# Performance work log

Hardware: AMD Instinct MI355X
Metric: run time of the kernel (lower is better)

Reference implementation:

```python
import jax, jax.numpy as jnp
import numpy as np

NUM_ATOMS = 100
D = 32        # initial_atom_dim
H = 16        # hidden_dim (multiplicity per irrep)
NB = 16       # edge_dim / number of bessel basis functions
CUT = 6.0     # radius_cutoff
DEG = 4.0     # degree_norm
OUT = 1       # output_dim
INV4PI = 1.0 / np.sqrt(4.0 * np.pi)  # 'integral' SH normalization


def _bessel(d, nb, cut):
    # e3nn soft_one_hot_linspace(basis='bessel', cutoff=True) * sqrt(nb)
    x = d[:, None]
    n = jnp.arange(1, nb + 1, dtype=d.dtype)
    safe = jnp.maximum(x, 1e-9)
    out = np.sqrt(2.0 / cut) * jnp.sin(n * jnp.pi * x / cut) / safe
    return out * (x < cut) * np.sqrt(float(nb))


def _fc(x, w1, w2):
    # e3nn FullyConnectedNet: fan-in normalized linear layers, silu, no bias
    h = jax.nn.silu(x @ w1 / np.sqrt(x.shape[-1]))
    return h @ w2 / np.sqrt(w1.shape[-1])


def _forward(atomic_numbers, edge_index, coords, atom_emb,
             fc0_w1, fc0_w2, fc1_w1, fc1_w2, w_readout):
    src, dst = edge_index[0], edge_index[1]
    N = coords.shape[0]
    E = src.shape[0]

    vec = coords[src] - coords[dst]                      # [E,3]
    dist = jnp.linalg.norm(vec, axis=-1)                 # [E]
    unit = vec / jnp.maximum(dist, 1e-9)[:, None]

    # spherical harmonics, l=0 and l=1, 'integral' normalization
    y0 = jnp.full((E,), INV4PI, dtype=coords.dtype)      # [E]
    y1 = (np.sqrt(3.0) * INV4PI) * unit                  # [E,3]
    basis = _bessel(dist, NB, CUT)                       # [E,NB]

    x = atom_emb[atomic_numbers]                         # [N,D] (row 0 is padding)

    # ---- layer 0: scalars (D x0e) x (1x0e+1x1o) -> H x0e + H x1o ----
    w = _fc(basis, fc0_w1, fc0_w2)                       # [E, 2*D*H] per-edge TP weights
    wa = w[:, : D * H].reshape(E, D, H)
    wb = w[:, D * H:].reshape(E, D, H)
    xs = x[src]
    n0 = 1.0 / np.sqrt(D)                                # path fan-in norm
    m0 = jnp.einsum('ed,edh->eh', xs, wa) * y0[:, None] * n0          # [E,H]
    m1 = jnp.einsum('ed,edh->eh', xs, wb)[:, :, None] * y1[:, None, :] * n0  # [E,H,3]
    z0 = jax.ops.segment_sum(m0, dst, num_segments=N) / DEG           # [N,H]
    z1 = jax.ops.segment_sum(m1, dst, num_segments=N) / DEG           # [N,H,3]

    # ---- layer 1: (H x0e + H x1o) x (1x0e+1x1o) -> same irreps, skip-connected ----
    w = _fc(basis, fc1_w1, fc1_w2)                       # [E, 4*H*H]
    w1_ = w[:, 0 * H * H:1 * H * H].reshape(E, H, H)     # 0e x 0e -> 0e
    w2_ = w[:, 1 * H * H:2 * H * H].reshape(E, H, H)     # 0e x 1o -> 1o
    w3_ = w[:, 2 * H * H:3 * H * H].reshape(E, H, H)     # 1o x 0e -> 1o
    w4_ = w[:, 3 * H * H:4 * H * H].reshape(E, H, H)     # 1o x 1o -> 0e (CG = dot/sqrt(3))
    s, v = z0[src], z1[src]
    n1 = 1.0 / np.sqrt(2 * H)                            # two paths per output irrep
    dot = jnp.einsum('ehm,em->eh', v, y1) / np.sqrt(3.0)
    o0 = (jnp.einsum('eh,ehk->ek', s, w1_) * y0[:, None]
          + jnp.einsum('eh,ehk->ek', dot, w4_)) * n1
    o1 = (jnp.einsum('eh,ehk->ek', s, w2_)[:, :, None] * y1[:, None, :]
          + jnp.einsum('ehm,ehk->ekm', v, w3_) * y0[:, None, None]) * n1
    z0 = jax.ops.segment_sum(o0, dst, num_segments=N) / DEG + z0      # skip
    z1 = jax.ops.segment_sum(o1, dst, num_segments=N) / DEG + z1

    # ---- scalar readout (o3.Linear onto 0e) + graph sum-pool ----
    node_scalar = z0 @ w_readout / np.sqrt(H)            # [N,OUT]
    return jnp.sum(node_scalar, axis=0)                  # [OUT]


def setup_inputs() -> dict:
    key = jax.random.key(0)
    ks = jax.random.split(key, 9)
    N, E = 10000, 160000
    atomic_numbers = jax.random.randint(ks[0], (N,), 0, NUM_ATOMS)
    coords = jax.random.normal(ks[1], (N, 3), dtype=jnp.float32)
    edge_index = jax.random.randint(ks[2], (2, E), 0, N)
    atom_emb = jax.random.normal(ks[3], (NUM_ATOMS, D), dtype=jnp.float32).at[0].set(0.0)
    fc0_w1 = jax.random.normal(ks[4], (NB, H), dtype=jnp.float32)
    fc0_w2 = jax.random.normal(ks[5], (H, 2 * D * H), dtype=jnp.float32)
    fc1_w1 = jax.random.normal(ks[6], (NB, H), dtype=jnp.float32)
    fc1_w2 = jax.random.normal(ks[7], (H, 4 * H * H), dtype=jnp.float32)
    w_readout = jax.random.normal(ks[8], (H, OUT), dtype=jnp.float32)
    return {"atomic_numbers": atomic_numbers, "coords": coords, "edge_index": edge_index,
            "atom_emb": atom_emb, "fc0_w1": fc0_w1, "fc0_w2": fc0_w2,
            "fc1_w1": fc1_w1, "fc1_w2": fc1_w2, "w_readout": w_readout}


def reference(atomic_numbers, coords, edge_index, atom_emb,
              fc0_w1, fc0_w2, fc1_w1, fc1_w2, w_readout):
    return _forward(atomic_numbers, edge_index, coords, atom_emb,
                    fc0_w1, fc0_w2, fc1_w1, fc1_w2, w_readout)
```

## Files before the change

kernel.cpp:

```cpp
#include <hip/hip_runtime.h>
#include <math.h>


namespace {
constexpr int   NATOMS   = 100;
constexpr int   CAP      = 64;
constexpr float PI_F     = 3.14159265358979323846f;
constexpr float INV4PI_F = 0.28209479177387814f;
constexpr float SQRT3_F  = 1.7320508075688772f;
constexpr float CUT_F    = 6.0f;
constexpr float BASIS_C  = 2.3094010767585034f;
constexpr float N0_F     = 0.17677669529663687f;
constexpr float K0_F = INV4PI_F * N0_F * 0.0625f;
constexpr float K1_F = SQRT3_F * INV4PI_F * N0_F * 0.0625f;
constexpr float P2SC = INV4PI_F * N0_F * (1.0f / 64.0f);
}

__device__ __forceinline__ float silu_fast(float x) {
  return x / (1.0f + __expf(-x));
}

__device__ __forceinline__ float block_reduce_sum(float v) {
  #pragma unroll
  for (int o = 32; o > 0; o >>= 1) v += __shfl_down(v, o, 64);
  __shared__ float ls[8];
  int lane = threadIdx.x & 63;
  int w    = threadIdx.x >> 6;
  if (lane == 0) ls[w] = v;
  __syncthreads();
  float s = 0.f;
  if (threadIdx.x == 0) {
    int nw = (blockDim.x + 63) >> 6;
    for (int i = 0; i < nw; ++i) s += ls[i];
  }
  return s;
}

__global__ void table_kernel(const float* __restrict__ atom_emb,
                             const float* __restrict__ fc0_w2,
                             const float* __restrict__ fc1_w2,
                             const float* __restrict__ w_readout,
                             float* __restrict__ TI,
                             float* __restrict__ G1T, float* __restrict__ G4T) {
  int b = blockIdx.x;
  int tt = threadIdx.x;
  int j = tt >> 4;
  int h = tt & 15;
  if (b < NATOMS) {
    float s0 = 0.f, s1 = 0.f;
    #pragma unroll
    for (int d = 0; d < 32; ++d) {
      float x = atom_emb[b * 32 + d];
      s0 = fmaf(x, fc0_w2[j * 1024 + d * 16 + h], s0);
      s1 = fmaf(x, fc0_w2[j * 1024 + 512 + d * 16 + h], s1);
    }
    TI[b * 512 + j * 32 + 2 * h]     = s0;
    TI[b * 512 + j * 32 + 2 * h + 1] = s1;
  } else {
    float g1 = 0.f, g4 = 0.f;
    #pragma unroll
    for (int k = 0; k < 16; ++k) {
      float r = w_readout[k];
      g1 = fmaf(fc1_w2[j * 1024 + h * 16 + k], r, g1);
      g4 = fmaf(fc1_w2[j * 1024 + 768 + h * 16 + k], r, g4);
    }
    G1T[h * 16 + j] = g1;
    G4T[h * 16 + j] = g4;
  }
}

__global__ void __launch_bounds__(256)
edge_kernel(const int* __restrict__ ei,
            const float* __restrict__ coords,
            const int* __restrict__ an,
            const float* __restrict__ TI,
            const float* __restrict__ fc0_w1,
            const float* __restrict__ fc1_w1,
            int* __restrict__ dcur, int* __restrict__ scur,
            float2* __restrict__ mbuf,
            float4* __restrict__ ubuf,
            float4* __restrict__ sbuf,
            float* __restrict__ hbuf,
            int E) {
  int lane = threadIdx.x & 63;
  int g    = threadIdx.x >> 4;
  int t    = threadIdx.x & 15;
  int base = lane & 48;

  float w0c[16], w1c[16];
  #pragma unroll
  for (int k = 0; k < 16; ++k) {
    w0c[k] = fc0_w1[k * 16 + t];
    w1c[k] = fc1_w1[k * 16 + t];
  }

  const float angc = PI_F / CUT_F;
  int e = blockIdx.x * 32 + g;
  #pragma unroll
  for (int rep = 0; rep < 2; ++rep, e += 16) {
    if (e < E) {
      int s = ei[e];
      int d = ei[E + e];
      float vx = coords[3 * s + 0] - coords[3 * d + 0];
      float vy = coords[3 * s + 1] - coords[3 * d + 1];
      float vz = coords[3 * s + 2] - coords[3 * d + 2];
      float dist = sqrtf(vx * vx + vy * vy + vz * vz);
      float inv  = 1.0f / fmaxf(dist, 1e-9f);
      float ux = vx * inv, uy = vy * inv, uz = vz * inv;
      float bc = (dist < CUT_F) ? (BASIS_C * inv) : 0.0f;

      int dslotv = 0, sslotv = 0;
      if (t == 0) {
        float4 rec = make_float4(ux, uy, uz, dist);
        int pos  = atomicAdd(&dcur[d], 1);
        int spos = atomicAdd(&scur[s], 1);
        int dslot = d * CAP + min(pos, CAP - 1);
        int sslot = s * CAP + min(spos, CAP - 1);
        ubuf[dslot] = rec;
        sbuf[sslot] = rec;
        dslotv = dslot; sslotv = sslot;
      }
      int dslot = __shfl(dslotv, base, 64);
      int sslot = __shfl(sslotv, base, 64);

      float ang = angc * dist;
      float sc0 = __sinf(ang);
      float tw  = 2.0f * __cosf(ang);
      float sc1 = sc0;
      float sp0 = 0.f, sp1 = 0.f, acc0 = 0.f, acc1 = 0.f;
      #pragma unroll
      for (int k = 0; k < 16; ++k) {
        acc0 = fmaf(sc0, w0c[k], acc0);
        acc1 = fmaf(sc1, w1c[k], acc1);
        float sn0 = fmaf(tw, sc0, -sp0); sp0 = sc0; sc0 = sn0;
        float sn1 = fmaf(tw, sc1, -sp1); sp1 = sc1; sc1 = sn1;
      }
      float h0t = silu_fast(acc0 * bc * 0.25f);
      float h1t = silu_fast(acc1 * bc * 0.25f);

      hbuf[(size_t)sslot * 16 + t] = h1t;

      int a = an[s];
      const float2* tp = (const float2*)(TI + a * 512) + t;
      float u0 = 0.f, u1 = 0.f;
      #pragma unroll
      for (int j = 0; j < 16; ++j) {
        float hj = __shfl(h0t, base + j, 64);
        float2 T = tp[j * 16];
        u0 = fmaf(hj, T.x, u0);
        u1 = fmaf(hj, T.y, u1);
      }
      mbuf[(size_t)dslot * 16 + t] = make_float2(K0_F * u0, K1_F * u1);
    }
  }
}

__global__ void __launch_bounds__(256, 4)
node_kernel(const int* __restrict__ dcur,
            const int* __restrict__ scur,
            const float2* __restrict__ mbuf,
            const float4* __restrict__ ubuf,
            const float4* __restrict__ sbuf,
            const float* __restrict__ hbuf,
            const float* __restrict__ G1T,
            const float* __restrict__ G4T,
            const float* __restrict__ w_readout,
            float* __restrict__ out,
            int N) {
  __shared__ float ggs[512];
  ggs[threadIdx.x]       = G1T[threadIdx.x];
  ggs[256 + threadIdx.x] = G4T[threadIdx.x];
  __syncthreads();

  int wave = threadIdx.x >> 6;
  int lane = threadIdx.x & 63;
  int g    = lane >> 4;
  int t    = lane & 15;
  int base = lane & 48;
  int node = blockIdx.x * 4 + wave;
  bool valid = node < N;

  float rr = w_readout[t];
  int cin  = valid ? min(dcur[node], CAP) : 0;
  int cout = valid ? min(scur[node], CAP) : 0;
  size_t nb = (size_t)(valid ? node : 0) * CAP;

  float a0 = 0.f, ax = 0.f, ay = 0.f, az = 0.f;
  for (int i = g; i < cin; i += 4) {
    float2 f  = mbuf[(nb + i) * 16 + t];
    float4 uu = ubuf[nb + i];
    a0 += f.x;
    ax = fmaf(f.y, uu.x, ax);
    ay = fmaf(f.y, uu.y, ay);
    az = fmaf(f.y, uu.z, az);
  }
  a0 += __shfl_xor(a0, 16, 64); a0 += __shfl_xor(a0, 32, 64);
  ax += __shfl_xor(ax, 16, 64); ax += __shfl_xor(ax, 32, 64);
  ay += __shfl_xor(ay, 16, 64); ay += __shfl_xor(ay, 32, 64);
  az += __shfl_xor(az, 16, 64); az += __shfl_xor(az, 32, 64);

  float srcv = (g == 0) ? a0 : ((g == 1) ? ax : (g == 2) ? ay : az);
  int tofs = (g == 0) ? 0 : 256;
  float o = 0.f;
  #pragma unroll
  for (int h = 0; h < 16; ++h) {
    float vh = __shfl(srcv, base + h, 64);
    o = fmaf(ggs[tofs + h * 16 + t], vh, o);
  }
  float Qt  = __shfl(o, t, 64);
  float Pxt = __shfl(o, 16 + t, 64);
  float Pyt = __shfl(o, 32 + t, 64);
  float Pzt = __shfl(o, 48 + t, 64);

  float c = 0.f;
  for (int i = g; i < cout; i += 4) {
    float h1 = hbuf[(nb + i) * 16 + t];
    float4 uu = sbuf[nb + i];
    c = fmaf(h1, fmaf(Pxt, uu.x, fmaf(Pyt, uu.y, fmaf(Pzt, uu.z, Qt))), c);
  }
  c *= P2SC;
  if (valid && g == 0) c = fmaf(a0 * rr, 0.25f, c);
  if (!valid) c = 0.f;

  float tot = block_reduce_sum(c);
  if (threadIdx.x == 0) atomicAdd(out, tot);
}

extern "C" void kernel_launch(void* const* d_in, const int* in_sizes, int n_in,
                              void* d_out, int out_size, void* d_ws, size_t ws_size,
                              hipStream_t stream) {
  const int*   an        = (const int*)d_in[0];
  const float* coords    = (const float*)d_in[1];
  const int*   ei        = (const int*)d_in[2];
  const float* atom_emb  = (const float*)d_in[3];
  const float* fc0_w1    = (const float*)d_in[4];
  const float* fc0_w2    = (const float*)d_in[5];
  const float* fc1_w1    = (const float*)d_in[6];
  const float* fc1_w2    = (const float*)d_in[7];
  const float* w_readout = (const float*)d_in[8];

  int N = in_sizes[0];
  int E = in_sizes[2] / 2;
  size_t slots = (size_t)N * CAP;

  float4* ubuf = (float4*)d_ws;
  float4* sbuf = ubuf + slots;
  float2* mbuf = (float2*)(sbuf + slots);
  float*  hbuf = (float*)(mbuf + slots * 16);
  float*  TI   = hbuf + slots * 16;
  float*  G1T  = TI + NATOMS * 512;
  float*  G4T  = G1T + 256;
  int*    dcur = (int*)(G4T + 256);
  int*    scur = dcur + N;
  float*  out = (float*)d_out;

  hipMemsetAsync(dcur, 0, (size_t)2 * N * sizeof(int), stream);
  hipMemsetAsync(out, 0, sizeof(float), stream);

  int blk = 256;
  table_kernel<<<NATOMS + 1, blk, 0, stream>>>(
      atom_emb, fc0_w2, fc1_w2, w_readout, TI, G1T, G4T);

  edge_kernel<<<(E + 31) / 32, blk, 0, stream>>>(
      ei, coords, an, TI, fc0_w1, fc1_w1, dcur, scur,
      mbuf, ubuf, sbuf, hbuf, E);

  node_kernel<<<(N + 3) / 4, blk, 0, stream>>>(
      dcur, scur, mbuf, ubuf, sbuf, hbuf, G1T, G4T, w_readout, out, N);
}
```

Measured before the change: 150.9 us.

## Fold memsets into table kernel and interleave two edges per thread

Removes the two hipMemsetAsync calls by having extra blocks of the table kernel zero the per-node counters and the output scalar, which saves launch overhead. The edge kernel is restructured so each thread issues the loads, atomics and math for both of its edges together instead of looping over them one at a time. This exposes more memory-level parallelism and hides gather latency, at the cost of more registers per thread.

```diff
diff --git a/kernel.cpp b/kernel.cpp
--- a/kernel.cpp
+++ b/kernel.cpp
@@ -41,12 +41,15 @@
                              const float* __restrict__ fc1_w2,
                              const float* __restrict__ w_readout,
                              float* __restrict__ TI,
-                             float* __restrict__ G1T, float* __restrict__ G4T) {
+                             float* __restrict__ G1T, float* __restrict__ G4T,
+                             int* __restrict__ dcur,
+                             float* __restrict__ out,
+                             int N2) {
   int b = blockIdx.x;
   int tt = threadIdx.x;
-  int j = tt >> 4;
-  int h = tt & 15;
   if (b < NATOMS) {
+    int j = tt >> 4;
+    int h = tt & 15;
     float s0 = 0.f, s1 = 0.f;
     #pragma unroll
     for (int d = 0; d < 32; ++d) {
@@ -56,7 +59,9 @@
     }
     TI[b * 512 + j * 32 + 2 * h]     = s0;
     TI[b * 512 + j * 32 + 2 * h + 1] = s1;
-  } else {
+  } else if (b == NATOMS) {
+    int j = tt >> 4;
+    int h = tt & 15;
     float g1 = 0.f, g4 = 0.f;
     #pragma unroll
     for (int k = 0; k < 16; ++k) {
@@ -66,6 +71,10 @@
     }
     G1T[h * 16 + j] = g1;
     G4T[h * 16 + j] = g4;
+    if (tt == 0) *out = 0.f;
+  } else {
+    int idx = (b - NATOMS - 1) * 256 + tt;
+    if (idx < N2) dcur[idx] = 0;
   }
 }
 
@@ -95,63 +104,93 @@
   }
 
   const float angc = PI_F / CUT_F;
-  int e = blockIdx.x * 32 + g;
-  #pragma unroll
-  for (int rep = 0; rep < 2; ++rep, e += 16) {
-    if (e < E) {
-      int s = ei[e];
-      int d = ei[E + e];
-      float vx = coords[3 * s + 0] - coords[3 * d + 0];
-      float vy = coords[3 * s + 1] - coords[3 * d + 1];
-      float vz = coords[3 * s + 2] - coords[3 * d + 2];
-      float dist = sqrtf(vx * vx + vy * vy + vz * vz);
-      float inv  = 1.0f / fmaxf(dist, 1e-9f);
-      float ux = vx * inv, uy = vy * inv, uz = vz * inv;
-      float bc = (dist < CUT_F) ? (BASIS_C * inv) : 0.0f;
-
-      int dslotv = 0, sslotv = 0;
-      if (t == 0) {
-        float4 rec = make_float4(ux, uy, uz, dist);
-        int pos  = atomicAdd(&dcur[d], 1);
-        int spos = atomicAdd(&scur[s], 1);
-        int dslot = d * CAP + min(pos, CAP - 1);
-        int sslot = s * CAP + min(spos, CAP - 1);
-        ubuf[dslot] = rec;
-        sbuf[sslot] = rec;
-        dslotv = dslot; sslotv = sslot;
-      }
-      int dslot = __shfl(dslotv, base, 64);
-      int sslot = __shfl(sslotv, base, 64);
-
-      float ang = angc * dist;
-      float sc0 = __sinf(ang);
-      float tw  = 2.0f * __cosf(ang);
-      float sc1 = sc0;
-      float sp0 = 0.f, sp1 = 0.f, acc0 = 0.f, acc1 = 0.f;
-      #pragma unroll
-      for (int k = 0; k < 16; ++k) {
-        acc0 = fmaf(sc0, w0c[k], acc0);
-        acc1 = fmaf(sc1, w1c[k], acc1);
-        float sn0 = fmaf(tw, sc0, -sp0); sp0 = sc0; sc0 = sn0;
-        float sn1 = fmaf(tw, sc1, -sp1); sp1 = sc1; sc1 = sn1;
-      }
-      float h0t = silu_fast(acc0 * bc * 0.25f);
-      float h1t = silu_fast(acc1 * bc * 0.25f);
-
-      hbuf[(size_t)sslot * 16 + t] = h1t;
-
-      int a = an[s];
-      const float2* tp = (const float2*)(TI + a * 512) + t;
-      float u0 = 0.f, u1 = 0.f;
-      #pragma unroll
-      for (int j = 0; j < 16; ++j) {
-        float hj = __shfl(h0t, base + j, 64);
-        float2 T = tp[j * 16];
-        u0 = fmaf(hj, T.x, u0);
-        u1 = fmaf(hj, T.y, u1);
-      }
-      mbuf[(size_t)dslot * 16 + t] = make_float2(K0_F * u0, K1_F * u1);
+  int eA = blockIdx.x * 32 + g;
+  int eB = eA + 16;
+  bool vA = eA < E, vB = eB < E;
+  int eAc = vA ? eA : 0, eBc = vB ? eB : 0;
+
+  int sA = ei[eAc], dA = ei[E + eAc];
+  int sB = ei[eBc], dB = ei[E + eBc];
+  float sxA = coords[3 * sA + 0], syA = coords[3 * sA + 1], szA = coords[3 * sA + 2];
+  float dxA = coords[3 * dA + 0], dyA = coords[3 * dA + 1], dzA = coords[3 * dA + 2];
+  float sxB = coords[3 * sB + 0], syB = coords[3 * sB + 1], szB = coords[3 * sB + 2];
+  float dxB = coords[3 * dB + 0], dyB = coords[3 * dB + 1], dzB = coords[3 * dB + 2];
+  int aA = an[sA], aB = an[sB];
+
+  float vxA = sxA - dxA, vyA = syA - dyA, vzA = szA - dzA;
+  float vxB = sxB - dxB, vyB = syB - dyB, vzB = szB - dzB;
+  float distA = sqrtf(vxA * vxA + vyA * vyA + vzA * vzA);
+  float distB = sqrtf(vxB * vxB + vyB * vyB + vzB * vzB);
+  float ivA = 1.0f / fmaxf(distA, 1e-9f);
+  float ivB = 1.0f / fmaxf(distB, 1e-9f);
+  float uxA = vxA * ivA, uyA = vyA * ivA, uzA = vzA * ivA;
+  float uxB = vxB * ivB, uyB = vyB * ivB, uzB = vzB * ivB;
+  float bcA = (distA < CUT_F) ? (BASIS_C * ivA) : 0.0f;
+  float bcB = (distB < CUT_F) ? (BASIS_C * ivB) : 0.0f;
+
+  int dsAv = 0, ssAv = 0, dsBv = 0, ssBv = 0;
+  if (t == 0) {
+    if (vA) {
+      int p = atomicAdd(&dcur[dA], 1), q = atomicAdd(&scur[sA], 1);
+      dsAv = dA * CAP + min(p, CAP - 1);
+      ssAv = sA * CAP + min(q, CAP - 1);
+      ubuf[dsAv] = make_float4(uxA, uyA, uzA, distA);
+      sbuf[ssAv] = make_float4(uxA, uyA, uzA, distA);
     }
+    if (vB) {
+      int p = atomicAdd(&dcur[dB], 1), q = atomicAdd(&scur[sB], 1);
+      dsBv = dB * CAP + min(p, CAP - 1);
+      ssBv = sB * CAP + min(q, CAP - 1);
+      ubuf[dsBv] = make_float4(uxB, uyB, uzB, distB);
+      sbuf[ssBv] = make_float4(uxB, uyB, uzB, distB);
+    }
+  }
+
+  float angA = angc * distA, angB = angc * distB;
+  float scA = __sinf(angA), twA = 2.0f * __cosf(angA), spA = 0.f;
+  float scB = __sinf(angB), twB = 2.0f * __cosf(angB), spB = 0.f;
+  float a0A = 0.f, a1A = 0.f, a0B = 0.f, a1B = 0.f;
+  #pragma unroll
+  for (int k = 0; k < 16; ++k) {
+    a0A = fmaf(scA, w0c[k], a0A);
+    a1A = fmaf(scA, w1c[k], a1A);
+    a0B = fmaf(scB, w0c[k], a0B);
+    a1B = fmaf(scB, w1c[k], a1B);
+    float snA = fmaf(twA, scA, -spA); spA = scA; scA = snA;
+    float snB = fmaf(twB, scB, -spB); spB = scB; scB = snB;
+  }
+  float h0A = silu_fast(a0A * bcA * 0.25f);
+  float h1A = silu_fast(a1A * bcA * 0.25f);
+  float h0B = silu_fast(a0B * bcB * 0.25f);
+  float h1B = silu_fast(a1B * bcB * 0.25f);
+
+  int dsA = __shfl(dsAv, base, 64);
+  int ssA = __shfl(ssAv, base, 64);
+  int dsB = __shfl(dsBv, base, 64);
+  int ssB = __shfl(ssBv, base, 64);
+
+  const float2* tpA = (const float2*)(TI + aA * 512) + t;
+  const float2* tpB = (const float2*)(TI + aB * 512) + t;
+  float u0A = 0.f, u1A = 0.f, u0B = 0.f, u1B = 0.f;
+  #pragma unroll
+  for (int j = 0; j < 16; ++j) {
+    float hjA = __shfl(h0A, base + j, 64);
+    float hjB = __shfl(h0B, base + j, 64);
+    float2 TA = tpA[j * 16];
+    float2 TB = tpB[j * 16];
+    u0A = fmaf(hjA, TA.x, u0A);
+    u1A = fmaf(hjA, TA.y, u1A);
+    u0B = fmaf(hjB, TB.x, u0B);
+    u1B = fmaf(hjB, TB.y, u1B);
+  }
+
+  if (vA) {
+    hbuf[(size_t)ssA * 16 + t] = h1A;
+    mbuf[(size_t)dsA * 16 + t] = make_float2(K0_F * u0A, K1_F * u1A);
+  }
+  if (vB) {
+    hbuf[(size_t)ssB * 16 + t] = h1B;
+    mbuf[(size_t)dsB * 16 + t] = make_float2(K0_F * u0B, K1_F * u1B);
   }
 }
 
@@ -254,12 +293,10 @@
   int*    scur = dcur + N;
   float*  out = (float*)d_out;
 
-  hipMemsetAsync(dcur, 0, (size_t)2 * N * sizeof(int), stream);
-  hipMemsetAsync(out, 0, sizeof(float), stream);
-
   int blk = 256;
-  table_kernel<<<NATOMS + 1, blk, 0, stream>>>(
-      atom_emb, fc0_w2, fc1_w2, w_readout, TI, G1T, G4T);
+  int zgrid = (2 * N + blk - 1) / blk;
+  table_kernel<<<NATOMS + 1 + zgrid, blk, 0, stream>>>(
+      atom_emb, fc0_w2, fc1_w2, w_readout, TI, G1T, G4T, dcur, out, 2 * N);
 
   edge_kernel<<<(E + 31) / 32, blk, 0, stream>>>(
       ei, coords, an, TI, fc0_w1, fc1_w1, dcur, scur,
```

After: 149.1 us. About the same (-1.2%).

## Fold readout projections into per-atom tables and drop node-side matvec

Applied to the files above, without the earlier changes.

Precomputes per-atom tables that already include the readout projections (G1/G4 and w_readout) and the constant scale factors, so the node kernel no longer does a 16x16 shuffle matvec per node. The scalar readout term moves into the edge kernel as a per-block reduction with an atomic add. The two memsets are replaced by zeroing blocks inside the table kernel, and the first-layer weights are transposed so the edge kernel can load them as float4. This adds one block reduction and one atomic per edge block.

```diff
diff --git a/kernel.cpp b/kernel.cpp
--- a/kernel.cpp
+++ b/kernel.cpp
@@ -40,32 +40,63 @@
                              const float* __restrict__ fc0_w2,
                              const float* __restrict__ fc1_w2,
                              const float* __restrict__ w_readout,
-                             float* __restrict__ TI,
-                             float* __restrict__ G1T, float* __restrict__ G4T) {
+                             const float* __restrict__ fc0_w1,
+                             const float* __restrict__ fc1_w1,
+                             float* __restrict__ TQP,
+                             float* __restrict__ TR,
+                             float* __restrict__ W0T,
+                             float* __restrict__ W1T,
+                             int* __restrict__ dcur,
+                             float* __restrict__ out,
+                             int N2) {
   int b = blockIdx.x;
   int tt = threadIdx.x;
-  int j = tt >> 4;
-  int h = tt & 15;
   if (b < NATOMS) {
-    float s0 = 0.f, s1 = 0.f;
+    __shared__ float ls0[256], ls1[256], lgq[256], lg4[256];
+    int k = tt >> 4;
+    int h = tt & 15;
+    float t0 = 0.f, t1 = 0.f;
     #pragma unroll
     for (int d = 0; d < 32; ++d) {
       float x = atom_emb[b * 32 + d];
-      s0 = fmaf(x, fc0_w2[j * 1024 + d * 16 + h], s0);
-      s1 = fmaf(x, fc0_w2[j * 1024 + 512 + d * 16 + h], s1);
-    }
-    TI[b * 512 + j * 32 + 2 * h]     = s0;
-    TI[b * 512 + j * 32 + 2 * h + 1] = s1;
+      t0 = fmaf(x, fc0_w2[k * 1024 + d * 16 + h], t0);
+      t1 = fmaf(x, fc0_w2[k * 1024 + 512 + d * 16 + h], t1);
+    }
+    ls0[tt] = t0;
+    ls1[tt] = t1;
+    int h2 = tt >> 4, j2 = tt & 15;
+    float g1 = 0.f, g4 = 0.f;
+    #pragma unroll
+    for (int s = 0; s < 16; ++s) {
+      float r = w_readout[s];
+      g1 = fmaf(fc1_w2[j2 * 1024 + h2 * 16 + s], r, g1);
+      g4 = fmaf(fc1_w2[j2 * 1024 + 768 + h2 * 16 + s], r, g4);
+    }
+    lgq[tt] = g1;
+    lg4[tt] = g4;
+    __syncthreads();
+    float tq = 0.f, tp = 0.f;
+    #pragma unroll
+    for (int s = 0; s < 16; ++s) {
+      tq = fmaf(lgq[s * 16 + h], ls0[k * 16 + s], tq);
+      tp = fmaf(lg4[s * 16 + h], ls1[k * 16 + s], tp);
+    }
+    TQP[b * 512 + k * 32 + 2 * h]     = K0_F * tq;
+    TQP[b * 512 + k * 32 + 2 * h + 1] = K1_F * tp;
+    if (h == 0) {
+      float tr = 0.f;
+      #pragma unroll
+      for (int s = 0; s < 16; ++s) tr = fmaf(w_readout[s], ls0[k * 16 + s], tr);
+      TR[b * 16 + k] = 0.25f * K0_F * tr;
+    }
+  } else if (b == NATOMS) {
+    int t = tt >> 4, k = tt & 15;
+    W0T[t * 16 + k] = fc0_w1[k * 16 + t];
+    W1T[t * 16 + k] = fc1_w1[k * 16 + t];
+    if (tt == 0) *out = 0.f;
   } else {
-    float g1 = 0.f, g4 = 0.f;
-    #pragma unroll
-    for (int k = 0; k < 16; ++k) {
-      float r = w_readout[k];
-      g1 = fmaf(fc1_w2[j * 1024 + h * 16 + k], r, g1);
-      g4 = fmaf(fc1_w2[j * 1024 + 768 + h * 16 + k], r, g4);
-    }
-    G1T[h * 16 + j] = g1;
-    G4T[h * 16 + j] = g4;
+    int idx = (b - NATOMS - 1) * 256 + tt;
+    if (idx < N2) dcur[idx] = 0;
   }
 }
 
@@ -73,14 +104,16 @@
 edge_kernel(const int* __restrict__ ei,
             const float* __restrict__ coords,
             const int* __restrict__ an,
-            const float* __restrict__ TI,
-            const float* __restrict__ fc0_w1,
-            const float* __restrict__ fc1_w1,
+            const float* __restrict__ TQP,
+            const float* __restrict__ TR,
+            const float* __restrict__ W0T,
+            const float* __restrict__ W1T,
             int* __restrict__ dcur, int* __restrict__ scur,
             float2* __restrict__ mbuf,
             float4* __restrict__ ubuf,
             float4* __restrict__ sbuf,
             float* __restrict__ hbuf,
+            float* __restrict__ out,
             int E) {
   int lane = threadIdx.x & 63;
   int g    = threadIdx.x >> 4;
@@ -88,13 +121,21 @@
   int base = lane & 48;
 
   float w0c[16], w1c[16];
-  #pragma unroll
-  for (int k = 0; k < 16; ++k) {
-    w0c[k] = fc0_w1[k * 16 + t];
-    w1c[k] = fc1_w1[k * 16 + t];
+  {
+    const float4* p0 = (const float4*)(W0T + t * 16);
+    const float4* p1 = (const float4*)(W1T + t * 16);
+    #pragma unroll
+    for (int q = 0; q < 4; ++q) {
+      float4 a = p0[q], b = p1[q];
+      w0c[q * 4 + 0] = a.x; w0c[q * 4 + 1] = a.y;
+      w0c[q * 4 + 2] = a.z; w0c[q * 4 + 3] = a.w;
+      w1c[q * 4 + 0] = b.x; w1c[q * 4 + 1] = b.y;
+      w1c[q * 4 + 2] = b.z; w1c[q * 4 + 3] = b.w;
+    }
   }
 
   const float angc = PI_F / CUT_F;
+  float roacc = 0.f;
   int e = blockIdx.x * 32 + g;
   #pragma unroll
   for (int rep = 0; rep < 2; ++rep, e += 16) {
@@ -112,47 +153,49 @@
       int dslotv = 0, sslotv = 0;
       if (t == 0) {
         float4 rec = make_float4(ux, uy, uz, dist);
-        int pos  = atomicAdd(&dcur[d], 1);
-        int spos = atomicAdd(&scur[s], 1);
-        int dslot = d * CAP + min(pos, CAP - 1);
-        int sslot = s * CAP + min(spos, CAP - 1);
-        ubuf[dslot] = rec;
-        sbuf[sslot] = rec;
-        dslotv = dslot; sslotv = sslot;
+        int p = atomicAdd(&dcur[d], 1);
+        int q = atomicAdd(&scur[s], 1);
+        dslotv = d * CAP + min(p, CAP - 1);
+        sslotv = s * CAP + min(q, CAP - 1);
+        ubuf[dslotv] = rec;
+        sbuf[sslotv] = rec;
       }
+
+      float ang = angc * dist;
+      float sc = __sinf(ang);
+      float tw = 2.0f * __cosf(ang);
+      float sp = 0.f, a0 = 0.f, a1 = 0.f;
+      #pragma unroll
+      for (int k = 0; k < 16; ++k) {
+        a0 = fmaf(sc, w0c[k], a0);
+        a1 = fmaf(sc, w1c[k], a1);
+        float sn = fmaf(tw, sc, -sp); sp = sc; sc = sn;
+      }
+      float h0t = silu_fast(a0 * bc * 0.25f);
+      float h1t = silu_fast(a1 * bc * 0.25f);
+
+      int a = an[s];
+      roacc = fmaf(h0t, TR[a * 16 + t], roacc);
+
       int dslot = __shfl(dslotv, base, 64);
       int sslot = __shfl(sslotv, base, 64);
 
-      float ang = angc * dist;
-      float sc0 = __sinf(ang);
-      float tw  = 2.0f * __cosf(ang);
-      float sc1 = sc0;
-      float sp0 = 0.f, sp1 = 0.f, acc0 = 0.f, acc1 = 0.f;
+      const float2* tp = (const float2*)(TQP + a * 512) + t;
+      float qv = 0.f, pv = 0.f;
       #pragma unroll
       for (int k = 0; k < 16; ++k) {
-        acc0 = fmaf(sc0, w0c[k], acc0);
-        acc1 = fmaf(sc1, w1c[k], acc1);
-        float sn0 = fmaf(tw, sc0, -sp0); sp0 = sc0; sc0 = sn0;
-        float sn1 = fmaf(tw, sc1, -sp1); sp1 = sc1; sc1 = sn1;
+        float hk = __shfl(h0t, base + k, 64);
+        float2 T = tp[k * 16];
+        qv = fmaf(hk, T.x, qv);
+        pv = fmaf(hk, T.y, pv);
       }
-      float h0t = silu_fast(acc0 * bc * 0.25f);
-      float h1t = silu_fast(acc1 * bc * 0.25f);
 
       hbuf[(size_t)sslot * 16 + t] = h1t;
-
-      int a = an[s];
-      const float2* tp = (const float2*)(TI + a * 512) + t;
-      float u0 = 0.f, u1 = 0.f;
-      #pragma unroll
-      for (int j = 0; j < 16; ++j) {
-        float hj = __shfl(h0t, base + j, 64);
-        float2 T = tp[j * 16];
-        u0 = fmaf(hj, T.x, u0);
-        u1 = fmaf(hj, T.y, u1);
-      }
-      mbuf[(size_t)dslot * 16 + t] = make_float2(K0_F * u0, K1_F * u1);
-    }
-  }
+      mbuf[(size_t)dslot * 16 + t] = make_float2(qv, pv);
+    }
+  }
+  float tot = block_reduce_sum(roacc);
+  if (threadIdx.x == 0) atomicAdd(out, tot);
 }
 
 __global__ void __launch_bounds__(256, 4)
@@ -162,64 +205,40 @@
             const float4* __restrict__ ubuf,
             const float4* __restrict__ sbuf,
             const float* __restrict__ hbuf,
-            const float* __restrict__ G1T,
-            const float* __restrict__ G4T,
-            const float* __restrict__ w_readout,
             float* __restrict__ out,
             int N) {
-  __shared__ float ggs[512];
-  ggs[threadIdx.x]       = G1T[threadIdx.x];
-  ggs[256 + threadIdx.x] = G4T[threadIdx.x];
-  __syncthreads();
-
   int wave = threadIdx.x >> 6;
   int lane = threadIdx.x & 63;
   int g    = lane >> 4;
   int t    = lane & 15;
-  int base = lane & 48;
   int node = blockIdx.x * 4 + wave;
   bool valid = node < N;
 
-  float rr = w_readout[t];
   int cin  = valid ? min(dcur[node], CAP) : 0;
   int cout = valid ? min(scur[node], CAP) : 0;
   size_t nb = (size_t)(valid ? node : 0) * CAP;
 
-  float a0 = 0.f, ax = 0.f, ay = 0.f, az = 0.f;
+  float aq = 0.f, ax = 0.f, ay = 0.f, az = 0.f;
   for (int i = g; i < cin; i += 4) {
     float2 f  = mbuf[(nb + i) * 16 + t];
     float4 uu = ubuf[nb + i];
-    a0 += f.x;
+    aq += f.x;
     ax = fmaf(f.y, uu.x, ax);
     ay = fmaf(f.y, uu.y, ay);
     az = fmaf(f.y, uu.z, az);
   }
-  a0 += __shfl_xor(a0, 16, 64); a0 += __shfl_xor(a0, 32, 64);
+  aq += __shfl_xor(aq, 16, 64); aq += __shfl_xor(aq, 32, 64);
   ax += __shfl_xor(ax, 16, 64); ax += __shfl_xor(ax, 32, 64);
   ay += __shfl_xor(ay, 16, 64); ay += __shfl_xor(ay, 32, 64);
   az += __shfl_xor(az, 16, 64); az += __shfl_xor(az, 32, 64);
-
-  float srcv = (g == 0) ? a0 : ((g == 1) ? ax : (g == 2) ? ay : az);
-  int tofs = (g == 0) ? 0 : 256;
-  float o = 0.f;
-  #pragma unroll
-  for (int h = 0; h < 16; ++h) {
-    float vh = __shfl(srcv, base + h, 64);
-    o = fmaf(ggs[tofs + h * 16 + t], vh, o);
-  }
-  float Qt  = __shfl(o, t, 64);
-  float Pxt = __shfl(o, 16 + t, 64);
-  float Pyt = __shfl(o, 32 + t, 64);
-  float Pzt = __shfl(o, 48 + t, 64);
 
   float c = 0.f;
   for (int i = g; i < cout; i += 4) {
     float h1 = hbuf[(nb + i) * 16 + t];
     float4 uu = sbuf[nb + i];
-    c = fmaf(h1, fmaf(Pxt, uu.x, fmaf(Pyt, uu.y, fmaf(Pzt, uu.z, Qt))), c);
+    c = fmaf(h1, fmaf(ax, uu.x, fmaf(ay, uu.y, fmaf(az, uu.z, aq))), c);
   }
   c *= P2SC;
-  if (valid && g == 0) c = fmaf(a0 * rr, 0.25f, c);
   if (!valid) c = 0.f;
 
   float tot = block_reduce_sum(c);
@@ -247,24 +266,24 @@
   float4* sbuf = ubuf + slots;
   float2* mbuf = (float2*)(sbuf + slots);
   float*  hbuf = (float*)(mbuf + slots * 16);
-  float*  TI   = hbuf + slots * 16;
-  float*  G1T  = TI + NATOMS * 512;
-  float*  G4T  = G1T + 256;
-  int*    dcur = (int*)(G4T + 256);
+  float*  TQP  = hbuf + slots * 16;
+  float*  TR   = TQP + NATOMS * 512;
+  float*  W0T  = TR + NATOMS * 16;
+  float*  W1T  = W0T + 256;
+  int*    dcur = (int*)(W1T + 256);
   int*    scur = dcur + N;
   float*  out = (float*)d_out;
 
-  hipMemsetAsync(dcur, 0, (size_t)2 * N * sizeof(int), stream);
-  hipMemsetAsync(out, 0, sizeof(float), stream);
-
   int blk = 256;
-  table_kernel<<<NATOMS + 1, blk, 0, stream>>>(
-      atom_emb, fc0_w2, fc1_w2, w_readout, TI, G1T, G4T);
+  int zgrid = (2 * N + blk - 1) / blk;
+  table_kernel<<<NATOMS + 1 + zgrid, blk, 0, stream>>>(
+      atom_emb, fc0_w2, fc1_w2, w_readout, fc0_w1, fc1_w1,
+      TQP, TR, W0T, W1T, dcur, out, 2 * N);
 
   edge_kernel<<<(E + 31) / 32, blk, 0, stream>>>(
-      ei, coords, an, TI, fc0_w1, fc1_w1, dcur, scur,
-      mbuf, ubuf, sbuf, hbuf, E);
+      ei, coords, an, TQP, TR, W0T, W1T, dcur, scur,
+      mbuf, ubuf, sbuf, hbuf, out, E);
 
   node_kernel<<<(N + 3) / 4, blk, 0, stream>>>(
-      dcur, scur, mbuf, ubuf, sbuf, hbuf, G1T, G4T, w_readout, out, N);
-}
+      dcur, scur, mbuf, ubuf, sbuf, hbuf, out, N);
+}
```

Result: slower. 188.7 us (+25.0%).
